# Optimization experiments

Hardware: AMD Instinct MI355X
Metric: run time of the kernel (lower is better)

## Reference

```python
import jax, jax.numpy as jnp
import numpy as np
from jax import lax

T, B, D_IN, H, D_OUT = 512, 64, 256, 512, 256


def _lstm_scan(xs, h0, c0, Wih, Whh, b):
    """Standard LSTM over time. xs: [T,B,Din]; returns (hs [T,B,H], hT, cT).
    Gate order i,f,g,o (PyTorch convention)."""
    def step(carry, x_t):
        h, c = carry
        gates = x_t @ Wih.T + h @ Whh.T + b            # [B, 4H]
        i, f, g, o = jnp.split(gates, 4, axis=-1)
        i = jax.nn.sigmoid(i)
        f = jax.nn.sigmoid(f)
        g = jnp.tanh(g)
        o = jax.nn.sigmoid(o)
        c = f * c + i * g
        h = o * jnp.tanh(c)
        return (h, c), h
    (hT, cT), hs = lax.scan(step, (h0, c0), xs)
    return hs, hT, cT


def setup_inputs() -> dict:
    key = jax.random.key(0)
    ks = jax.random.split(key, 10)
    s = 0.05
    return {
        "x": jax.random.normal(ks[0], (T, B, D_IN), jnp.float32),
        "target": jax.random.uniform(ks[1], (T, B, D_OUT), jnp.float32),
        "hidden_state": jnp.zeros((1, B, H), jnp.float32),
        "cell_state": jnp.zeros((1, B, H), jnp.float32),
        "enc_Wih": jax.random.normal(ks[2], (4 * H, D_IN), jnp.float32) * s,
        "enc_Whh": jax.random.normal(ks[3], (4 * H, H), jnp.float32) * s,
        "enc_b": jax.random.normal(ks[4], (4 * H,), jnp.float32) * s,
        "dec_Wih": jax.random.normal(ks[5], (4 * H, D_OUT), jnp.float32) * s,
        "dec_Whh": jax.random.normal(ks[6], (4 * H, H), jnp.float32) * s,
        "dec_b": jax.random.normal(ks[7], (4 * H,), jnp.float32) * s,
        "fc_W": jax.random.normal(ks[8], (D_OUT, H), jnp.float32) * s,
        "fc_b": jax.random.normal(ks[9], (D_OUT,), jnp.float32) * s,
    }


def reference(x, target, hidden_state, cell_state,
              enc_Wih, enc_Whh, enc_b, dec_Wih, dec_Whh, dec_b, fc_W, fc_b):
    # Encoder: consume x, keep final (h, c).
    _, h, c = _lstm_scan(x, hidden_state[0], cell_state[0], enc_Wih, enc_Whh, enc_b)
    # Decoder with teacher_forcing = 1.0: input at step t is target[t-1],
    # step 0 input is zeros (matches torch code's initial x = zeros).
    dec_in = jnp.concatenate([jnp.zeros((1,) + target.shape[1:], target.dtype),
                              target[:-1]], axis=0)          # [T, B, D_OUT]
    hs, _, _ = _lstm_scan(dec_in, h, c, dec_Wih, dec_Whh, dec_b)  # [T, B, H]
    logits = hs @ fc_W.T + fc_b                                   # [T, B, D_OUT]
    return jax.nn.softmax(logits, axis=-1)
```

## Files before the change

### kernel.cpp

```cpp
#include <hip/hip_runtime.h>
#include <math.h>

#define TT 512
#define BB 64
#define DIN 256
#define HH 512
#define DOUT 256

#define RSU 388
#define RSH 776
#define PST 68

#define A_HI_OFF 0
#define A_LO_OFF 6208
#define P_OFF    12416
#define B_OFF    14592
#define C_OFF    14656
#define HST_HI   14912
#define HST_LO   15040
#define SMEM_U32 15168
#define SMEM_BYTES (SMEM_U32*4)

#define FCS 516

typedef _Float16 f16x8 __attribute__((ext_vector_type(8)));
typedef float    f32x4 __attribute__((ext_vector_type(4)));
typedef unsigned u32x4 __attribute__((ext_vector_type(4)));

union H16 { _Float16 f; unsigned short u; };
__device__ __forceinline__ unsigned short f16bits(_Float16 h) { H16 t; t.f = h; return t.u; }

__device__ __forceinline__ void pack2(float x, float y, unsigned& hi, unsigned& lo) {
    _Float16 hx = (_Float16)x, hy = (_Float16)y;
    _Float16 lx = (_Float16)((x - (float)hx) * 2048.0f);
    _Float16 ly = (_Float16)((y - (float)hy) * 2048.0f);
    hi = (unsigned)f16bits(hx) | ((unsigned)f16bits(hy) << 16);
    lo = (unsigned)f16bits(lx) | ((unsigned)f16bits(ly) << 16);
}

__device__ __forceinline__ u32x4 ld16_cohere(const void* p) {
    u32x4 v;
    asm volatile("global_load_dwordx4 %0, %1, off sc0 sc1"
                 : "=&v"(v) : "v"(p) : "memory");
    return v;
}
__device__ __forceinline__ void st16_cohere(void* p, u32x4 v) {
    asm volatile("global_store_dwordx4 %0, %1, off sc0 sc1"
                 :: "v"(p), "v"(v) : "memory");
}

__device__ __forceinline__ bool tag_ok(u32x4 v, unsigned par) {
    unsigned a = v[0] & v[1] & v[2] & v[3];
    unsigned o = v[0] | v[1] | v[2] | v[3];
    unsigned x = par ? ~a : o;
    return (x & 0x00010001u) == 0u;
}

__device__ __forceinline__ void load_w_regs(const float* __restrict__ Whh,
                                            const float* __restrict__ Wih,
                                            int u0, int ct, int kh, int m, int q,
                                            f16x8 (&whi)[12], f16x8 (&wlo)[12]) {
    const int C = ct*HH + u0 + m;
    const float* rowH = Whh + (size_t)C*HH;
    const float* rowI = Wih + (size_t)C*DIN;
    #pragma unroll
    for (int j = 0; j < 12; ++j) {
        const int ks = kh*12 + j;
        const float* src = (ks < 16) ? (rowH + ks*32 + q*8)
                                     : (rowI + (ks - 16)*32 + q*8);
        float4 a = ((const float4*)src)[0];
        float4 b = ((const float4*)src)[1];
        f16x8 h8, l8; _Float16 t16;
        t16=(_Float16)a.x; h8[0]=t16; l8[0]=(_Float16)((a.x-(float)t16)*2048.0f);
        t16=(_Float16)a.y; h8[1]=t16; l8[1]=(_Float16)((a.y-(float)t16)*2048.0f);
        t16=(_Float16)a.z; h8[2]=t16; l8[2]=(_Float16)((a.z-(float)t16)*2048.0f);
        t16=(_Float16)a.w; h8[3]=t16; l8[3]=(_Float16)((a.w-(float)t16)*2048.0f);
        t16=(_Float16)b.x; h8[4]=t16; l8[4]=(_Float16)((b.x-(float)t16)*2048.0f);
        t16=(_Float16)b.y; h8[5]=t16; l8[5]=(_Float16)((b.y-(float)t16)*2048.0f);
        t16=(_Float16)b.z; h8[6]=t16; l8[6]=(_Float16)((b.z-(float)t16)*2048.0f);
        t16=(_Float16)b.w; h8[7]=t16; l8[7]=(_Float16)((b.w-(float)t16)*2048.0f);
        whi[j] = h8; wlo[j] = l8;
    }
}

__device__ __forceinline__ void stage_x_f16(unsigned* __restrict__ sm32,
                                            const float* __restrict__ src, int tid) {
    for (int r = 0; r < 2; ++r) {
        int idx4 = tid + 512*r;
        int b = idx4 >> 6, j4 = idx4 & 63;
        float4 v = ((const float4*)(src + (size_t)b*DIN))[j4];
        unsigned h0, l0, h1, l1;
        pack2(v.x, v.y, h0, l0);
        pack2(v.z, v.w, h1, l1);
        int o = b*RSU + 256 + 2*j4;
        sm32[A_HI_OFF + o]     = h0;
        sm32[A_HI_OFF + o + 1] = h1;
        sm32[A_LO_OFF + o]     = l0;
        sm32[A_LO_OFF + o + 1] = l1;
    }
}

__device__ __forceinline__ void stage_x_zero_f16(unsigned* __restrict__ sm32, int tid) {
    for (int r = 0; r < 2; ++r) {
        int idx = tid + 512*r;
        int row = idx >> 6, j = idx & 63;
        int o = row*RSU + 256 + 2*j;
        sm32[A_HI_OFF + o]     = 0u;
        sm32[A_HI_OFF + o + 1] = 0u;
        sm32[A_LO_OFF + o]     = 0u;
        sm32[A_LO_OFF + o + 1] = 0u;
    }
}

__global__ __launch_bounds__(512, 1)
void lstm_persist(const float* __restrict__ x, const float* __restrict__ target,
                  const float* __restrict__ h0, const float* __restrict__ c0,
                  const float* __restrict__ eWih, const float* __restrict__ eWhh,
                  const float* __restrict__ eb,
                  const float* __restrict__ dWih, const float* __restrict__ dWhh,
                  const float* __restrict__ db,
                  float* __restrict__ hs,
                  unsigned short* __restrict__ hbh,
                  unsigned short* __restrict__ hbl)
{
    extern __shared__ unsigned sm32[];
    float* p_l = (float*)(sm32 + P_OFF);
    float* b_l = (float*)(sm32 + B_OFF);
    float* c_l = (float*)(sm32 + C_OFF);
    unsigned* hst_hi = sm32 + HST_HI;
    unsigned* hst_lo = sm32 + HST_LO;

    const int tid = (int)threadIdx.x;
    const int g   = (int)(blockIdx.x & 3);
    const int ij  = (int)(blockIdx.x >> 2);
    const int b0  = g * 16;
    const int u0  = ij * 16;

    if (tid < 256) {
        int b = tid >> 4, u = tid & 15;
        c_l[tid] = c0[(size_t)(b0 + b)*HH + u0 + u];
    }
    if (tid < 64) b_l[tid] = eb[(tid >> 4)*HH + u0 + (tid & 15)];
    stage_x_f16(sm32, x + (size_t)b0*DIN, tid);
    for (int r = 0; r < 4; ++r) {
        int idx4 = tid + 512*r;
        int b = idx4 >> 7, j4 = idx4 & 127;
        float4 v = ((const float4*)(h0 + (size_t)(b0 + b)*HH))[j4];
        unsigned h0p, l0p, h1p, l1p;
        pack2(v.x, v.y, h0p, l0p);
        pack2(v.z, v.w, h1p, l1p);
        int o = b*RSU + 2*j4;
        sm32[A_HI_OFF + o]     = h0p;
        sm32[A_HI_OFF + o + 1] = h1p;
        sm32[A_LO_OFF + o]     = l0p;
        sm32[A_LO_OFF + o + 1] = l1p;
    }
    __syncthreads();

    const int lane = tid & 63;
    const int wid  = tid >> 6;
    const int m    = lane & 15;
    const int q    = lane >> 4;
    const int ct   = wid & 3;
    const int kh   = wid >> 2;

    const _Float16* aH = (const _Float16*)(sm32 + A_HI_OFF);
    const _Float16* aL = (const _Float16*)(sm32 + A_LO_OFF);
    const int abase = m*RSH + q*8 + (kh*12)*32;

    f16x8 whi[12], wlo[12];
    load_w_regs(eWhh, eWih, u0, ct, kh, m, q, whi, wlo);

    for (int s = 0; s < 1024; ++s) {
        f32x4 hh = {0.f,0.f,0.f,0.f}, hl = {0.f,0.f,0.f,0.f}, lh = {0.f,0.f,0.f,0.f};
        #pragma unroll
        for (int j = 0; j < 12; ++j) {
            f16x8 ah = *(const f16x8*)(aH + abase + j*32);
            f16x8 al = *(const f16x8*)(aL + abase + j*32);
            hh = __builtin_amdgcn_mfma_f32_16x16x32_f16(ah, whi[j], hh, 0, 0, 0);
            hl = __builtin_amdgcn_mfma_f32_16x16x32_f16(ah, wlo[j], hl, 0, 0, 0);
            lh = __builtin_amdgcn_mfma_f32_16x16x32_f16(al, whi[j], lh, 0, 0, 0);
        }
        {
            const float sc = 1.0f/2048.0f;
            float* pb = p_l + (kh*16 + q*4)*PST + ct*16 + m;
            #pragma unroll
            for (int i = 0; i < 4; ++i)
                pb[i*PST] = hh[i] + (hl[i] + lh[i])*sc;
        }
        __syncthreads();

        const unsigned par = (unsigned)(((s + 1) >> 1) & 1);

        float hval = 0.f;
        if (tid < 256) {
            const int b = tid >> 4, u = tid & 15;
            const float* p0 = p_l + (size_t)b*PST;
            const float* p1 = p_l + (size_t)(16 + b)*PST;
            float gi = b_l[u]      + p0[u]      + p1[u];
            float gf = b_l[16 + u] + p0[16 + u] + p1[16 + u];
            float gg = b_l[32 + u] + p0[32 + u] + p1[32 + u];
            float go = b_l[48 + u] + p0[48 + u] + p1[48 + u];
            float ii = 1.f/(1.f + expf(-gi));
            float ff = 1.f/(1.f + expf(-gf));
            float g2 = tanhf(gg);
            float oo = 1.f/(1.f + expf(-go));
            float c  = ff*c_l[tid] + ii*g2;
            c_l[tid] = c;
            hval = oo*tanhf(c);
            _Float16 hh16 = (_Float16)hval;
            unsigned uh = ((unsigned)f16bits(hh16) & 0xFFFEu) | par;
            H16 t16; t16.u = (unsigned short)uh;
            _Float16 hl16 = (_Float16)((hval - (float)t16.f) * 2048.0f);
            unsigned ul = ((unsigned)f16bits(hl16) & 0xFFFEu) | par;
            ((unsigned short*)hst_hi)[tid] = (unsigned short)uh;
            ((unsigned short*)hst_lo)[tid] = (unsigned short)ul;
        }
        __syncthreads();

        if (tid < 64) {
            asm volatile("s_waitcnt vmcnt(0)" ::: "memory");
            const int b = tid >> 2, part = tid & 3;
            const int isLo = part >> 1, h16 = part & 1;
            u32x4 v = *(const u32x4*)((isLo ? hst_lo : hst_hi) + b*8 + h16*4);
            unsigned short* base = (isLo ? hbl : hbh)
                + ((size_t)((s & 1) ^ 1)*BB + b0 + b)*HH + u0 + h16*8;
            st16_cohere(base, v);
        }

        if (s >= 512 && tid < 256) {
            int b = tid >> 4, u = tid & 15;
            hs[((size_t)(s - 512)*BB + (b0 + b))*HH + (u0 + u)] = hval;
        }
        if (s == 511) {
            load_w_regs(dWhh, dWih, u0, ct, kh, m, q, whi, wlo);
            if (tid < 64) b_l[tid] = db[(tid >> 4)*HH + u0 + (tid & 15)];
        }
        {
            int ns = s + 1;
            if (ns < 1024) {
                if (ns == 512)       stage_x_zero_f16(sm32, tid);
                else if (ns < 512)   stage_x_f16(sm32, x + ((size_t)ns*BB + b0)*DIN, tid);
                else                 stage_x_f16(sm32, target + ((size_t)(ns - 513)*BB + b0)*DOUT, tid);
            }
        }

        if (s < 1023) {
            const int slot = (s + 1) & 1;
            const u32x4* SH = (const u32x4*)(hbh + (size_t)slot*BB*HH + (size_t)b0*HH);
            const u32x4* SL = (const u32x4*)(hbl + (size_t)slot*BB*HH + (size_t)b0*HH);
            u32x4 v0 = {0,0,0,0}, v1 = {0,0,0,0}, v2 = {0,0,0,0}, v3 = {0,0,0,0};
            unsigned pend = 0xFu;
            do {
                if (pend & 1u) v0 = ld16_cohere(SH + tid);
                if (pend & 2u) v1 = ld16_cohere(SH + tid + 512);
                if (pend & 4u) v2 = ld16_cohere(SL + tid);
                if (pend & 8u) v3 = ld16_cohere(SL + tid + 512);
                asm volatile("s_waitcnt vmcnt(0)"
                             : "+v"(v0), "+v"(v1), "+v"(v2), "+v"(v3) :: "memory");
                if (tag_ok(v0, par)) pend &= ~1u;
                if (tag_ok(v1, par)) pend &= ~2u;
                if (tag_ok(v2, par)) pend &= ~4u;
                if (tag_ok(v3, par)) pend &= ~8u;
            } while (pend);
            const int j = tid & 63, r0 = tid >> 6;
            *(u32x4*)(sm32 + A_HI_OFF + (r0    )*RSU + j*4) = v0;
            *(u32x4*)(sm32 + A_HI_OFF + (r0 + 8)*RSU + j*4) = v1;
            *(u32x4*)(sm32 + A_LO_OFF + (r0    )*RSU + j*4) = v2;
            *(u32x4*)(sm32 + A_LO_OFF + (r0 + 8)*RSU + j*4) = v3;
        }
        __syncthreads();
    }
}

__global__ __launch_bounds__(256, 1)
void fc_kernel(const float* __restrict__ hs, const float* __restrict__ W,
               const float* __restrict__ bias, float* __restrict__ out)
{
    extern __shared__ float sm[];
    float* hs_l = sm;
    float* w_l  = sm + 16*FCS;

    const int tid = (int)threadIdx.x;
    const int rb = (int)(blockIdx.x >> 3);
    const int cb = (int)(blockIdx.x & 7);

    for (int r = 0; r < 8; ++r) {
        int id = tid + 256*r;
        int b = id >> 7, j = id & 127;
        float4 v = ((const float4*)(hs + (size_t)(rb*16 + b)*HH))[j];
        *(float4*)(hs_l + b*FCS + 4*j) = v;
    }
    for (int r = 0; r < 16; ++r) {
        int id = tid + 256*r;
        int c = id >> 7, j = id & 127;
        float4 v = ((const float4*)(W + (size_t)(cb*32 + c)*HH))[j];
        *(float4*)(w_l + c*FCS + 4*j) = v;
    }
    __syncthreads();

    const int kc = tid & 7, bt = (tid >> 3) & 3, ct = tid >> 5;
    float acc[4][4] = {};
    const float* ap = hs_l + (bt*4)*FCS + 4*kc;
    const float* wp = w_l  + (ct*4)*FCS + 4*kc;
    #pragma unroll 4
    for (int i = 0; i < 16; ++i) {
        float4 av[4], wv[4];
        #pragma unroll
        for (int q = 0; q < 4; ++q) av[q] = *(const float4*)(ap + q*FCS + 32*i);
        #pragma unroll
        for (int q = 0; q < 4; ++q) wv[q] = *(const float4*)(wp + q*FCS + 32*i);
        #pragma unroll
        for (int b2 = 0; b2 < 4; ++b2)
            #pragma unroll
            for (int c2 = 0; c2 < 4; ++c2)
                acc[b2][c2] += av[b2].x*wv[c2].x + av[b2].y*wv[c2].y
                             + av[b2].z*wv[c2].z + av[b2].w*wv[c2].w;
    }
    #pragma unroll
    for (int b2 = 0; b2 < 4; ++b2)
        #pragma unroll
        for (int c2 = 0; c2 < 4; ++c2) {
            float v = acc[b2][c2];
            v += __shfl_xor(v, 1, 64);
            v += __shfl_xor(v, 2, 64);
            v += __shfl_xor(v, 4, 64);
            acc[b2][c2] = v;
        }
    if (kc == 0) {
        #pragma unroll
        for (int b2 = 0; b2 < 4; ++b2)
            #pragma unroll
            for (int c2 = 0; c2 < 4; ++c2) {
                int row = rb*16 + bt*4 + b2;
                int col = cb*32 + ct*4 + c2;
                out[(size_t)row*DOUT + col] = acc[b2][c2] + bias[col];
            }
    }
}

__global__ __launch_bounds__(256, 1)
void softmax_kernel(float* __restrict__ out)
{
    int row  = (int)blockIdx.x * 4 + ((int)threadIdx.x >> 6);
    int lane = (int)threadIdx.x & 63;
    float4 v = ((const float4*)(out + (size_t)row*DOUT))[lane];
    float m = fmaxf(fmaxf(v.x, v.y), fmaxf(v.z, v.w));
    #pragma unroll
    for (int d = 1; d < 64; d <<= 1) m = fmaxf(m, __shfl_xor(m, d, 64));
    float ex = expf(v.x - m), ey = expf(v.y - m), ez = expf(v.z - m), ew = expf(v.w - m);
    float ssum = ex + ey + ez + ew;
    #pragma unroll
    for (int d = 1; d < 64; d <<= 1) ssum += __shfl_xor(ssum, d, 64);
    float inv = 1.f / ssum;
    float4 o = make_float4(ex*inv, ey*inv, ez*inv, ew*inv);
    ((float4*)(out + (size_t)row*DOUT))[lane] = o;
}

__global__ void init_kernel(unsigned* __restrict__ hbh32, unsigned* __restrict__ hbl32)
{
    int i = (int)blockIdx.x * 256 + (int)threadIdx.x;
    unsigned* base = (i < 8192) ? hbh32 : hbl32;
    int j = (i & 8191) * 4;
    unsigned val = (j < 16384) ? 0u : 0x00010001u;
    u32x4 v = {val, val, val, val};
    st16_cohere(base + j, v);
}

extern "C" void kernel_launch(void* const* d_in, const int* in_sizes, int n_in,
                              void* d_out, int out_size, void* d_ws, size_t ws_size,
                              hipStream_t stream) {
    (void)in_sizes; (void)n_in; (void)out_size; (void)ws_size;
    const float* x      = (const float*)d_in[0];
    const float* target = (const float*)d_in[1];
    const float* h0     = (const float*)d_in[2];
    const float* c0     = (const float*)d_in[3];
    const float* eWih   = (const float*)d_in[4];
    const float* eWhh   = (const float*)d_in[5];
    const float* eb     = (const float*)d_in[6];
    const float* dWih   = (const float*)d_in[7];
    const float* dWhh   = (const float*)d_in[8];
    const float* db     = (const float*)d_in[9];
    const float* fcW    = (const float*)d_in[10];
    const float* fcb    = (const float*)d_in[11];
    float* out = (float*)d_out;

    float* hs = (float*)d_ws + 1024;
    unsigned short* hbh = (unsigned short*)(hs + (size_t)TT*BB*HH);
    unsigned short* hbl = hbh + (size_t)2*BB*HH;

    init_kernel<<<dim3(64), dim3(256), 0, stream>>>((unsigned*)hbh, (unsigned*)hbl);

    lstm_persist<<<dim3(128), dim3(512), SMEM_BYTES, stream>>>(
        x, target, h0, c0, eWih, eWhh, eb, dWih, dWhh, db, hs, hbh, hbl);

    size_t lds_fc = (size_t)(48*FCS) * sizeof(float);
    fc_kernel<<<dim3(16384), dim3(256), lds_fc, stream>>>(hs, fcW, fcb, out);

    softmax_kernel<<<dim3(8192), dim3(256), 0, stream>>>(out);
}
```

Baseline: 4.013 ms.

## Overlap input-projection MFMAs with cross-block hidden-state wait; shuffle-based h publish

Reorders the per-step K split so each wave first runs the MFMAs for the x-input columns, which do not depend on the previous hidden state. Only then does it spin on the cross-block hidden-state exchange and run the recurrent columns. This hides part of the inter-block synchronisation latency behind independent tensor work. The hidden-state publish now packs values with wave shuffles and stores straight from registers, removing an LDS staging buffer and one __syncthreads per step. The restructured barrier placement and the parity handling must stay correct across blocks.

Measured after the change: 4.173 ms. +4.0%, slower.

```diff
diff --git a/kernel.cpp b/kernel.cpp
--- a/kernel.cpp
+++ b/kernel.cpp
@@ -16,9 +16,7 @@
 #define P_OFF    12416
 #define B_OFF    14592
 #define C_OFF    14656
-#define HST_HI   14912
-#define HST_LO   15040
-#define SMEM_U32 15168
+#define SMEM_U32 14912
 #define SMEM_BYTES (SMEM_U32*4)
 
 #define FCS 516
@@ -64,8 +62,8 @@
     const float* rowH = Whh + (size_t)C*HH;
     const float* rowI = Wih + (size_t)C*DIN;
     #pragma unroll
-    for (int j = 0; j < 12; ++j) {
-        const int ks = kh*12 + j;
+    for (int jj = 0; jj < 12; ++jj) {
+        const int ks = (jj < 8) ? (kh*8 + jj) : (16 + kh*4 + (jj - 8));
         const float* src = (ks < 16) ? (rowH + ks*32 + q*8)
                                      : (rowI + (ks - 16)*32 + q*8);
         float4 a = ((const float4*)src)[0];
@@ -79,7 +77,7 @@
         t16=(_Float16)b.y; h8[5]=t16; l8[5]=(_Float16)((b.y-(float)t16)*2048.0f);
         t16=(_Float16)b.z; h8[6]=t16; l8[6]=(_Float16)((b.z-(float)t16)*2048.0f);
         t16=(_Float16)b.w; h8[7]=t16; l8[7]=(_Float16)((b.w-(float)t16)*2048.0f);
-        whi[j] = h8; wlo[j] = l8;
+        whi[jj] = h8; wlo[jj] = l8;
     }
 }
 
@@ -127,8 +125,6 @@
     float* p_l = (float*)(sm32 + P_OFF);
     float* b_l = (float*)(sm32 + B_OFF);
     float* c_l = (float*)(sm32 + C_OFF);
-    unsigned* hst_hi = sm32 + HST_HI;
-    unsigned* hst_lo = sm32 + HST_LO;
 
     const int tid = (int)threadIdx.x;
     const int g   = (int)(blockIdx.x & 3);
@@ -166,7 +162,7 @@
 
     const _Float16* aH = (const _Float16*)(sm32 + A_HI_OFF);
     const _Float16* aL = (const _Float16*)(sm32 + A_LO_OFF);
-    const int abase = m*RSH + q*8 + (kh*12)*32;
+    const int abase = m*RSH + q*8;
 
     f16x8 whi[12], wlo[12];
     load_w_regs(eWhh, eWih, u0, ct, kh, m, q, whi, wlo);
@@ -174,12 +170,50 @@
     for (int s = 0; s < 1024; ++s) {
         f32x4 hh = {0.f,0.f,0.f,0.f}, hl = {0.f,0.f,0.f,0.f}, lh = {0.f,0.f,0.f,0.f};
         #pragma unroll
-        for (int j = 0; j < 12; ++j) {
-            f16x8 ah = *(const f16x8*)(aH + abase + j*32);
-            f16x8 al = *(const f16x8*)(aL + abase + j*32);
-            hh = __builtin_amdgcn_mfma_f32_16x16x32_f16(ah, whi[j], hh, 0, 0, 0);
-            hl = __builtin_amdgcn_mfma_f32_16x16x32_f16(ah, wlo[j], hl, 0, 0, 0);
-            lh = __builtin_amdgcn_mfma_f32_16x16x32_f16(al, whi[j], lh, 0, 0, 0);
+        for (int jj = 8; jj < 12; ++jj) {
+            const int ks = 16 + kh*4 + (jj - 8);
+            f16x8 ah = *(const f16x8*)(aH + abase + ks*32);
+            f16x8 al = *(const f16x8*)(aL + abase + ks*32);
+            hh = __builtin_amdgcn_mfma_f32_16x16x32_f16(ah, whi[jj], hh, 0, 0, 0);
+            hl = __builtin_amdgcn_mfma_f32_16x16x32_f16(ah, wlo[jj], hl, 0, 0, 0);
+            lh = __builtin_amdgcn_mfma_f32_16x16x32_f16(al, whi[jj], lh, 0, 0, 0);
+        }
+
+        if (s > 0) {
+            const int slot = s & 1;
+            const unsigned par2 = (unsigned)((s >> 1) & 1);
+            const u32x4* SH = (const u32x4*)(hbh + (size_t)slot*BB*HH + (size_t)b0*HH);
+            const u32x4* SL = (const u32x4*)(hbl + (size_t)slot*BB*HH + (size_t)b0*HH);
+            u32x4 v0 = {0,0,0,0}, v1 = {0,0,0,0}, v2 = {0,0,0,0}, v3 = {0,0,0,0};
+            unsigned pend = 0xFu;
+            do {
+                if (pend & 1u) v0 = ld16_cohere(SH + tid);
+                if (pend & 2u) v1 = ld16_cohere(SH + tid + 512);
+                if (pend & 4u) v2 = ld16_cohere(SL + tid);
+                if (pend & 8u) v3 = ld16_cohere(SL + tid + 512);
+                asm volatile("s_waitcnt vmcnt(0)"
+                             : "+v"(v0), "+v"(v1), "+v"(v2), "+v"(v3) :: "memory");
+                if (tag_ok(v0, par2)) pend &= ~1u;
+                if (tag_ok(v1, par2)) pend &= ~2u;
+                if (tag_ok(v2, par2)) pend &= ~4u;
+                if (tag_ok(v3, par2)) pend &= ~8u;
+            } while (pend);
+            const int j = tid & 63, r0 = tid >> 6;
+            *(u32x4*)(sm32 + A_HI_OFF + (r0    )*RSU + j*4) = v0;
+            *(u32x4*)(sm32 + A_HI_OFF + (r0 + 8)*RSU + j*4) = v1;
+            *(u32x4*)(sm32 + A_LO_OFF + (r0    )*RSU + j*4) = v2;
+            *(u32x4*)(sm32 + A_LO_OFF + (r0 + 8)*RSU + j*4) = v3;
+            __syncthreads();
+        }
+
+        #pragma unroll
+        for (int jj = 0; jj < 8; ++jj) {
+            const int ks = kh*8 + jj;
+            f16x8 ah = *(const f16x8*)(aH + abase + ks*32);
+            f16x8 al = *(const f16x8*)(aL + abase + ks*32);
+            hh = __builtin_amdgcn_mfma_f32_16x16x32_f16(ah, whi[jj], hh, 0, 0, 0);
+            hl = __builtin_amdgcn_mfma_f32_16x16x32_f16(ah, wlo[jj], hl, 0, 0, 0);
+            lh = __builtin_amdgcn_mfma_f32_16x16x32_f16(al, whi[jj], lh, 0, 0, 0);
         }
         {
             const float sc = 1.0f/2048.0f;
@@ -213,19 +247,22 @@
             H16 t16; t16.u = (unsigned short)uh;
             _Float16 hl16 = (_Float16)((hval - (float)t16.f) * 2048.0f);
             unsigned ul = ((unsigned)f16bits(hl16) & 0xFFFEu) | par;
-            ((unsigned short*)hst_hi)[tid] = (unsigned short)uh;
-            ((unsigned short*)hst_lo)[tid] = (unsigned short)ul;
-        }
-        __syncthreads();
-
-        if (tid < 64) {
+
             asm volatile("s_waitcnt vmcnt(0)" ::: "memory");
-            const int b = tid >> 2, part = tid & 3;
-            const int isLo = part >> 1, h16 = part & 1;
-            u32x4 v = *(const u32x4*)((isLo ? hst_lo : hst_hi) + b*8 + h16*4);
-            unsigned short* base = (isLo ? hbl : hbh)
-                + ((size_t)((s & 1) ^ 1)*BB + b0 + b)*HH + u0 + h16*8;
-            st16_cohere(base, v);
+            unsigned r0h = uh | (__shfl_xor(uh, 1, 64) << 16);
+            unsigned r0l = ul | (__shfl_xor(ul, 1, 64) << 16);
+            u32x4 vh, vl;
+            vh[0] = r0h; vh[1] = __shfl_xor(r0h, 2, 64);
+            vh[2] = __shfl_xor(r0h, 4, 64); vh[3] = __shfl_xor(r0h, 6, 64);
+            vl[0] = r0l; vl[1] = __shfl_xor(r0l, 2, 64);
+            vl[2] = __shfl_xor(r0l, 4, 64); vl[3] = __shfl_xor(r0l, 6, 64);
+            if ((u & 7) == 0) {
+                const int h16 = u >> 3;
+                size_t off = (size_t)((s & 1) ^ 1)*BB*HH
+                           + (size_t)(b0 + b)*HH + u0 + h16*8;
+                st16_cohere(hbh + off, vh);
+                st16_cohere(hbl + off, vl);
+            }
         }
 
         if (s >= 512 && tid < 256) {
@@ -243,31 +280,6 @@
                 else if (ns < 512)   stage_x_f16(sm32, x + ((size_t)ns*BB + b0)*DIN, tid);
                 else                 stage_x_f16(sm32, target + ((size_t)(ns - 513)*BB + b0)*DOUT, tid);
             }
-        }
-
-        if (s < 1023) {
-            const int slot = (s + 1) & 1;
-            const u32x4* SH = (const u32x4*)(hbh + (size_t)slot*BB*HH + (size_t)b0*HH);
-            const u32x4* SL = (const u32x4*)(hbl + (size_t)slot*BB*HH + (size_t)b0*HH);
-            u32x4 v0 = {0,0,0,0}, v1 = {0,0,0,0}, v2 = {0,0,0,0}, v3 = {0,0,0,0};
-            unsigned pend = 0xFu;
-            do {
-                if (pend & 1u) v0 = ld16_cohere(SH + tid);
-                if (pend & 2u) v1 = ld16_cohere(SH + tid + 512);
-                if (pend & 4u) v2 = ld16_cohere(SL + tid);
-                if (pend & 8u) v3 = ld16_cohere(SL + tid + 512);
-                asm volatile("s_waitcnt vmcnt(0)"
-                             : "+v"(v0), "+v"(v1), "+v"(v2), "+v"(v3) :: "memory");
-                if (tag_ok(v0, par)) pend &= ~1u;
-                if (tag_ok(v1, par)) pend &= ~2u;
-                if (tag_ok(v2, par)) pend &= ~4u;
-                if (tag_ok(v3, par)) pend &= ~8u;
-            } while (pend);
-            const int j = tid & 63, r0 = tid >> 6;
-            *(u32x4*)(sm32 + A_HI_OFF + (r0    )*RSU + j*4) = v0;
-            *(u32x4*)(sm32 + A_HI_OFF + (r0 + 8)*RSU + j*4) = v1;
-            *(u32x4*)(sm32 + A_LO_OFF + (r0    )*RSU + j*4) = v2;
-            *(u32x4*)(sm32 + A_LO_OFF + (r0 + 8)*RSU + j*4) = v3;
         }
         __syncthreads();
     }
```

## Load recurrent h directly into MFMA operands from global, overlapping x-projection with wait

Applied to the files above, without the earlier changes.

Each wave is repartitioned to cover all four gates over a slice of the K dimension. The wave now polls the tagged h exchange buffer from global memory straight into MFMA operand registers and consumes each half as soon as it is ready, instead of having the whole block wait, copy into LDS and sync. The x-input projection is issued before the poll so it overlaps the cross-block wait. The hi*lo MFMA products are folded into one accumulator, h0 initialisation moves into the init kernel, and the gate reduction now sums eight partials instead of two. The risk is extra wave-level spinning and global-load latency sitting on the critical path of every step.

Measured after the change: 4.358 ms. +8.6%, slower.

```diff
diff --git a/kernel.cpp b/kernel.cpp
--- a/kernel.cpp
+++ b/kernel.cpp
@@ -7,18 +7,18 @@
 #define HH 512
 #define DOUT 256
 
-#define RSU 388
-#define RSH 776
-#define PST 68
-
-#define A_HI_OFF 0
-#define A_LO_OFF 6208
-#define P_OFF    12416
-#define B_OFF    14592
-#define C_OFF    14656
-#define HST_HI   14912
-#define HST_LO   15040
-#define SMEM_U32 15168
+#define RSXU 132
+#define RSXH 264
+#define PST  68
+
+#define AXH_OFF 0
+#define AXL_OFF 2112
+#define P_OFF   4224
+#define B_OFF   12928
+#define C_OFF   12992
+#define HST_HI  13248
+#define HST_LO  13376
+#define SMEM_U32 13504
 #define SMEM_BYTES (SMEM_U32*4)
 
 #define FCS 516
@@ -27,7 +27,8 @@
 typedef float    f32x4 __attribute__((ext_vector_type(4)));
 typedef unsigned u32x4 __attribute__((ext_vector_type(4)));
 
-union H16 { _Float16 f; unsigned short u; };
+union H16  { _Float16 f; unsigned short u; };
+union V16  { u32x4 u; f16x8 f; };
 __device__ __forceinline__ unsigned short f16bits(_Float16 h) { H16 t; t.f = h; return t.u; }
 
 __device__ __forceinline__ void pack2(float x, float y, unsigned& hi, unsigned& lo) {
@@ -48,6 +49,10 @@
     asm volatile("global_store_dwordx4 %0, %1, off sc0 sc1"
                  :: "v"(p), "v"(v) : "memory");
 }
+__device__ __forceinline__ void st32_cohere(unsigned* p, unsigned v) {
+    asm volatile("global_store_dword %0, %1, off sc0 sc1"
+                 :: "v"(p), "v"(v) : "memory");
+}
 
 __device__ __forceinline__ bool tag_ok(u32x4 v, unsigned par) {
     unsigned a = v[0] & v[1] & v[2] & v[3];
@@ -58,28 +63,30 @@
 
 __device__ __forceinline__ void load_w_regs(const float* __restrict__ Whh,
                                             const float* __restrict__ Wih,
-                                            int u0, int ct, int kh, int m, int q,
-                                            f16x8 (&whi)[12], f16x8 (&wlo)[12]) {
-    const int C = ct*HH + u0 + m;
-    const float* rowH = Whh + (size_t)C*HH;
-    const float* rowI = Wih + (size_t)C*DIN;
+                                            int u0, int w, int m, int q,
+                                            f16x8 (&whi)[4][3], f16x8 (&wlo)[4][3]) {
     #pragma unroll
-    for (int j = 0; j < 12; ++j) {
-        const int ks = kh*12 + j;
-        const float* src = (ks < 16) ? (rowH + ks*32 + q*8)
-                                     : (rowI + (ks - 16)*32 + q*8);
-        float4 a = ((const float4*)src)[0];
-        float4 b = ((const float4*)src)[1];
-        f16x8 h8, l8; _Float16 t16;
-        t16=(_Float16)a.x; h8[0]=t16; l8[0]=(_Float16)((a.x-(float)t16)*2048.0f);
-        t16=(_Float16)a.y; h8[1]=t16; l8[1]=(_Float16)((a.y-(float)t16)*2048.0f);
-        t16=(_Float16)a.z; h8[2]=t16; l8[2]=(_Float16)((a.z-(float)t16)*2048.0f);
-        t16=(_Float16)a.w; h8[3]=t16; l8[3]=(_Float16)((a.w-(float)t16)*2048.0f);
-        t16=(_Float16)b.x; h8[4]=t16; l8[4]=(_Float16)((b.x-(float)t16)*2048.0f);
-        t16=(_Float16)b.y; h8[5]=t16; l8[5]=(_Float16)((b.y-(float)t16)*2048.0f);
-        t16=(_Float16)b.z; h8[6]=t16; l8[6]=(_Float16)((b.z-(float)t16)*2048.0f);
-        t16=(_Float16)b.w; h8[7]=t16; l8[7]=(_Float16)((b.w-(float)t16)*2048.0f);
-        whi[j] = h8; wlo[j] = l8;
+    for (int g = 0; g < 4; ++g) {
+        const int C = g*HH + u0 + m;
+        const float* rowH = Whh + (size_t)C*HH;
+        const float* rowI = Wih + (size_t)C*DIN;
+        #pragma unroll
+        for (int sl = 0; sl < 3; ++sl) {
+            const float* src = (sl < 2) ? (rowH + (2*w + sl)*32 + q*8)
+                                        : (rowI + w*32 + q*8);
+            float4 a = ((const float4*)src)[0];
+            float4 b = ((const float4*)src)[1];
+            f16x8 h8, l8; _Float16 t16;
+            t16=(_Float16)a.x; h8[0]=t16; l8[0]=(_Float16)((a.x-(float)t16)*2048.0f);
+            t16=(_Float16)a.y; h8[1]=t16; l8[1]=(_Float16)((a.y-(float)t16)*2048.0f);
+            t16=(_Float16)a.z; h8[2]=t16; l8[2]=(_Float16)((a.z-(float)t16)*2048.0f);
+            t16=(_Float16)a.w; h8[3]=t16; l8[3]=(_Float16)((a.w-(float)t16)*2048.0f);
+            t16=(_Float16)b.x; h8[4]=t16; l8[4]=(_Float16)((b.x-(float)t16)*2048.0f);
+            t16=(_Float16)b.y; h8[5]=t16; l8[5]=(_Float16)((b.y-(float)t16)*2048.0f);
+            t16=(_Float16)b.z; h8[6]=t16; l8[6]=(_Float16)((b.z-(float)t16)*2048.0f);
+            t16=(_Float16)b.w; h8[7]=t16; l8[7]=(_Float16)((b.w-(float)t16)*2048.0f);
+            whi[g][sl] = h8; wlo[g][sl] = l8;
+        }
     }
 }
 
@@ -92,11 +99,11 @@
         unsigned h0, l0, h1, l1;
         pack2(v.x, v.y, h0, l0);
         pack2(v.z, v.w, h1, l1);
-        int o = b*RSU + 256 + 2*j4;
-        sm32[A_HI_OFF + o]     = h0;
-        sm32[A_HI_OFF + o + 1] = h1;
-        sm32[A_LO_OFF + o]     = l0;
-        sm32[A_LO_OFF + o + 1] = l1;
+        int o = b*RSXU + 2*j4;
+        sm32[AXH_OFF + o]     = h0;
+        sm32[AXH_OFF + o + 1] = h1;
+        sm32[AXL_OFF + o]     = l0;
+        sm32[AXL_OFF + o + 1] = l1;
     }
 }
 
@@ -104,17 +111,17 @@
     for (int r = 0; r < 2; ++r) {
         int idx = tid + 512*r;
         int row = idx >> 6, j = idx & 63;
-        int o = row*RSU + 256 + 2*j;
-        sm32[A_HI_OFF + o]     = 0u;
-        sm32[A_HI_OFF + o + 1] = 0u;
-        sm32[A_LO_OFF + o]     = 0u;
-        sm32[A_LO_OFF + o + 1] = 0u;
+        int o = row*RSXU + 2*j;
+        sm32[AXH_OFF + o]     = 0u;
+        sm32[AXH_OFF + o + 1] = 0u;
+        sm32[AXL_OFF + o]     = 0u;
+        sm32[AXL_OFF + o + 1] = 0u;
     }
 }
 
 __global__ __launch_bounds__(512, 1)
 void lstm_persist(const float* __restrict__ x, const float* __restrict__ target,
-                  const float* __restrict__ h0, const float* __restrict__ c0,
+                  const float* __restrict__ c0,
                   const float* __restrict__ eWih, const float* __restrict__ eWhh,
                   const float* __restrict__ eb,
                   const float* __restrict__ dWih, const float* __restrict__ dWhh,
@@ -142,77 +149,117 @@
     }
     if (tid < 64) b_l[tid] = eb[(tid >> 4)*HH + u0 + (tid & 15)];
     stage_x_f16(sm32, x + (size_t)b0*DIN, tid);
-    for (int r = 0; r < 4; ++r) {
-        int idx4 = tid + 512*r;
-        int b = idx4 >> 7, j4 = idx4 & 127;
-        float4 v = ((const float4*)(h0 + (size_t)(b0 + b)*HH))[j4];
-        unsigned h0p, l0p, h1p, l1p;
-        pack2(v.x, v.y, h0p, l0p);
-        pack2(v.z, v.w, h1p, l1p);
-        int o = b*RSU + 2*j4;
-        sm32[A_HI_OFF + o]     = h0p;
-        sm32[A_HI_OFF + o + 1] = h1p;
-        sm32[A_LO_OFF + o]     = l0p;
-        sm32[A_LO_OFF + o + 1] = l1p;
-    }
     __syncthreads();
 
     const int lane = tid & 63;
     const int wid  = tid >> 6;
     const int m    = lane & 15;
     const int q    = lane >> 4;
-    const int ct   = wid & 3;
-    const int kh   = wid >> 2;
-
-    const _Float16* aH = (const _Float16*)(sm32 + A_HI_OFF);
-    const _Float16* aL = (const _Float16*)(sm32 + A_LO_OFF);
-    const int abase = m*RSH + q*8 + (kh*12)*32;
-
-    f16x8 whi[12], wlo[12];
-    load_w_regs(eWhh, eWih, u0, ct, kh, m, q, whi, wlo);
+
+    f16x8 whi[4][3], wlo[4][3];
+    load_w_regs(eWhh, eWih, u0, wid, m, q, whi, wlo);
+
+    const _Float16* aXH = (const _Float16*)(sm32 + AXH_OFF);
+    const _Float16* aXL = (const _Float16*)(sm32 + AXL_OFF);
+    const int xoff = m*RSXH + wid*32 + q*8;
+    const int o0 = wid*64 + q*8;
+    const int o1 = o0 + 32;
 
     for (int s = 0; s < 1024; ++s) {
-        f32x4 hh = {0.f,0.f,0.f,0.f}, hl = {0.f,0.f,0.f,0.f}, lh = {0.f,0.f,0.f,0.f};
-        #pragma unroll
-        for (int j = 0; j < 12; ++j) {
-            f16x8 ah = *(const f16x8*)(aH + abase + j*32);
-            f16x8 al = *(const f16x8*)(aL + abase + j*32);
-            hh = __builtin_amdgcn_mfma_f32_16x16x32_f16(ah, whi[j], hh, 0, 0, 0);
-            hl = __builtin_amdgcn_mfma_f32_16x16x32_f16(ah, wlo[j], hl, 0, 0, 0);
-            lh = __builtin_amdgcn_mfma_f32_16x16x32_f16(al, whi[j], lh, 0, 0, 0);
-        }
+        const int gslot = s & 1;
+        const unsigned gpar = (unsigned)((s >> 1) & 1);
+
+        f32x4 ahh[4], alo[4];
+        #pragma unroll
+        for (int gg = 0; gg < 4; ++gg) {
+            ahh[gg] = (f32x4){0.f,0.f,0.f,0.f};
+            alo[gg] = (f32x4){0.f,0.f,0.f,0.f};
+        }
+
+        {
+            f16x8 xh = *(const f16x8*)(aXH + xoff);
+            f16x8 xl = *(const f16x8*)(aXL + xoff);
+            #pragma unroll
+            for (int gg = 0; gg < 4; ++gg) {
+                ahh[gg] = __builtin_amdgcn_mfma_f32_16x16x32_f16(xh, whi[gg][2], ahh[gg], 0, 0, 0);
+                alo[gg] = __builtin_amdgcn_mfma_f32_16x16x32_f16(xl, whi[gg][2],
+                          __builtin_amdgcn_mfma_f32_16x16x32_f16(xh, wlo[gg][2], alo[gg], 0, 0, 0), 0, 0, 0);
+            }
+        }
+
+        {
+            const unsigned short* SH = hbh + (size_t)gslot*BB*HH + (size_t)(b0 + m)*HH;
+            const unsigned short* SL = hbl + (size_t)gslot*BB*HH + (size_t)(b0 + m)*HH;
+            u32x4 a0h = {0,0,0,0}, a0l = {0,0,0,0}, a1h = {0,0,0,0}, a1l = {0,0,0,0};
+            unsigned lp = 3u;
+            unsigned wp = 3u;
+            do {
+                if (lp & 1u) { a0h = ld16_cohere(SH + o0); a0l = ld16_cohere(SL + o0); }
+                if (lp & 2u) { a1h = ld16_cohere(SH + o1); a1l = ld16_cohere(SL + o1); }
+                asm volatile("s_waitcnt vmcnt(0)"
+                             : "+v"(a0h), "+v"(a0l), "+v"(a1h), "+v"(a1l) :: "memory");
+                if ((lp & 1u) && tag_ok(a0h, gpar) && tag_ok(a0l, gpar)) lp &= ~1u;
+                if ((lp & 2u) && tag_ok(a1h, gpar) && tag_ok(a1l, gpar)) lp &= ~2u;
+                if ((wp & 1u) && __all((lp & 1u) == 0u)) {
+                    V16 vh, vl; vh.u = a0h; vl.u = a0l;
+                    #pragma unroll
+                    for (int gg = 0; gg < 4; ++gg) {
+                        ahh[gg] = __builtin_amdgcn_mfma_f32_16x16x32_f16(vh.f, whi[gg][0], ahh[gg], 0, 0, 0);
+                        alo[gg] = __builtin_amdgcn_mfma_f32_16x16x32_f16(vl.f, whi[gg][0],
+                                  __builtin_amdgcn_mfma_f32_16x16x32_f16(vh.f, wlo[gg][0], alo[gg], 0, 0, 0), 0, 0, 0);
+                    }
+                    wp &= ~1u;
+                }
+                if ((wp & 2u) && __all((lp & 2u) == 0u)) {
+                    V16 vh, vl; vh.u = a1h; vl.u = a1l;
+                    #pragma unroll
+                    for (int gg = 0; gg < 4; ++gg) {
+                        ahh[gg] = __builtin_amdgcn_mfma_f32_16x16x32_f16(vh.f, whi[gg][1], ahh[gg], 0, 0, 0);
+                        alo[gg] = __builtin_amdgcn_mfma_f32_16x16x32_f16(vl.f, whi[gg][1],
+                                  __builtin_amdgcn_mfma_f32_16x16x32_f16(vh.f, wlo[gg][1], alo[gg], 0, 0, 0), 0, 0, 0);
+                    }
+                    wp &= ~2u;
+                }
+            } while (wp);
+        }
+
         {
             const float sc = 1.0f/2048.0f;
-            float* pb = p_l + (kh*16 + q*4)*PST + ct*16 + m;
+            float* pb = p_l + (wid*16 + q*4)*PST + m;
             #pragma unroll
-            for (int i = 0; i < 4; ++i)
-                pb[i*PST] = hh[i] + (hl[i] + lh[i])*sc;
+            for (int gg = 0; gg < 4; ++gg)
+                #pragma unroll
+                for (int i = 0; i < 4; ++i)
+                    pb[i*PST + gg*16] = ahh[gg][i] + alo[gg][i]*sc;
         }
         __syncthreads();
 
-        const unsigned par = (unsigned)(((s + 1) >> 1) & 1);
+        const unsigned ppar = (unsigned)(((s + 1) >> 1) & 1);
 
         float hval = 0.f;
         if (tid < 256) {
             const int b = tid >> 4, u = tid & 15;
-            const float* p0 = p_l + (size_t)b*PST;
-            const float* p1 = p_l + (size_t)(16 + b)*PST;
-            float gi = b_l[u]      + p0[u]      + p1[u];
-            float gf = b_l[16 + u] + p0[16 + u] + p1[16 + u];
-            float gg = b_l[32 + u] + p0[32 + u] + p1[32 + u];
-            float go = b_l[48 + u] + p0[48 + u] + p1[48 + u];
+            float gi = b_l[u], gf = b_l[16 + u], gg2 = b_l[32 + u], go = b_l[48 + u];
+            #pragma unroll
+            for (int w = 0; w < 8; ++w) {
+                const float* pp = p_l + (size_t)(w*16 + b)*PST;
+                gi  += pp[u];
+                gf  += pp[16 + u];
+                gg2 += pp[32 + u];
+                go  += pp[48 + u];
+            }
             float ii = 1.f/(1.f + expf(-gi));
             float ff = 1.f/(1.f + expf(-gf));
-            float g2 = tanhf(gg);
+            float g2 = tanhf(gg2);
             float oo = 1.f/(1.f + expf(-go));
             float c  = ff*c_l[tid] + ii*g2;
             c_l[tid] = c;
             hval = oo*tanhf(c);
             _Float16 hh16 = (_Float16)hval;
-            unsigned uh = ((unsigned)f16bits(hh16) & 0xFFFEu) | par;
+            unsigned uh = ((unsigned)f16bits(hh16) & 0xFFFEu) | ppar;
             H16 t16; t16.u = (unsigned short)uh;
             _Float16 hl16 = (_Float16)((hval - (float)t16.f) * 2048.0f);
-            unsigned ul = ((unsigned)f16bits(hl16) & 0xFFFEu) | par;
+            unsigned ul = ((unsigned)f16bits(hl16) & 0xFFFEu) | ppar;
             ((unsigned short*)hst_hi)[tid] = (unsigned short)uh;
             ((unsigned short*)hst_lo)[tid] = (unsigned short)ul;
         }
@@ -233,7 +280,7 @@
             hs[((size_t)(s - 512)*BB + (b0 + b))*HH + (u0 + u)] = hval;
         }
         if (s == 511) {
-            load_w_regs(dWhh, dWih, u0, ct, kh, m, q, whi, wlo);
+            load_w_regs(dWhh, dWih, u0, wid, m, q, whi, wlo);
             if (tid < 64) b_l[tid] = db[(tid >> 4)*HH + u0 + (tid & 15)];
         }
         {
@@ -243,31 +290,6 @@
                 else if (ns < 512)   stage_x_f16(sm32, x + ((size_t)ns*BB + b0)*DIN, tid);
                 else                 stage_x_f16(sm32, target + ((size_t)(ns - 513)*BB + b0)*DOUT, tid);
             }
-        }
-
-        if (s < 1023) {
-            const int slot = (s + 1) & 1;
-            const u32x4* SH = (const u32x4*)(hbh + (size_t)slot*BB*HH + (size_t)b0*HH);
-            const u32x4* SL = (const u32x4*)(hbl + (size_t)slot*BB*HH + (size_t)b0*HH);
-            u32x4 v0 = {0,0,0,0}, v1 = {0,0,0,0}, v2 = {0,0,0,0}, v3 = {0,0,0,0};
-            unsigned pend = 0xFu;
-            do {
-                if (pend & 1u) v0 = ld16_cohere(SH + tid);
-                if (pend & 2u) v1 = ld16_cohere(SH + tid + 512);
-                if (pend & 4u) v2 = ld16_cohere(SL + tid);
-                if (pend & 8u) v3 = ld16_cohere(SL + tid + 512);
-                asm volatile("s_waitcnt vmcnt(0)"
-                             : "+v"(v0), "+v"(v1), "+v"(v2), "+v"(v3) :: "memory");
-                if (tag_ok(v0, par)) pend &= ~1u;
-                if (tag_ok(v1, par)) pend &= ~2u;
-                if (tag_ok(v2, par)) pend &= ~4u;
-                if (tag_ok(v3, par)) pend &= ~8u;
-            } while (pend);
-            const int j = tid & 63, r0 = tid >> 6;
-            *(u32x4*)(sm32 + A_HI_OFF + (r0    )*RSU + j*4) = v0;
-            *(u32x4*)(sm32 + A_HI_OFF + (r0 + 8)*RSU + j*4) = v1;
-            *(u32x4*)(sm32 + A_LO_OFF + (r0    )*RSU + j*4) = v2;
-            *(u32x4*)(sm32 + A_LO_OFF + (r0 + 8)*RSU + j*4) = v3;
         }
         __syncthreads();
     }
@@ -357,14 +379,23 @@
     ((float4*)(out + (size_t)row*DOUT))[lane] = o;
 }
 
-__global__ void init_kernel(unsigned* __restrict__ hbh32, unsigned* __restrict__ hbl32)
+__global__ void init_kernel(const float* __restrict__ h0,
+                            unsigned* __restrict__ hbh32, unsigned* __restrict__ hbl32)
 {
     int i = (int)blockIdx.x * 256 + (int)threadIdx.x;
-    unsigned* base = (i < 8192) ? hbh32 : hbl32;
-    int j = (i & 8191) * 4;
-    unsigned val = (j < 16384) ? 0u : 0x00010001u;
-    u32x4 v = {val, val, val, val};
-    st16_cohere(base + j, v);
+    float x0 = h0[2*i], x1 = h0[2*i + 1];
+    _Float16 ha = (_Float16)x0;
+    unsigned ua = (unsigned)f16bits(ha) & 0xFFFEu;
+    H16 ta; ta.u = (unsigned short)ua;
+    unsigned la = (unsigned)f16bits((_Float16)((x0 - (float)ta.f)*2048.0f)) & 0xFFFEu;
+    _Float16 hb = (_Float16)x1;
+    unsigned ub = (unsigned)f16bits(hb) & 0xFFFEu;
+    H16 tb; tb.u = (unsigned short)ub;
+    unsigned lb = (unsigned)f16bits((_Float16)((x1 - (float)tb.f)*2048.0f)) & 0xFFFEu;
+    st32_cohere(hbh32 + i, ua | (ub << 16));
+    st32_cohere(hbl32 + i, la | (lb << 16));
+    st32_cohere(hbh32 + 16384 + i, 0x00010001u);
+    st32_cohere(hbl32 + 16384 + i, 0x00010001u);
 }
 
 extern "C" void kernel_launch(void* const* d_in, const int* in_sizes, int n_in,
@@ -389,10 +420,10 @@
     unsigned short* hbh = (unsigned short*)(hs + (size_t)TT*BB*HH);
     unsigned short* hbl = hbh + (size_t)2*BB*HH;
 
-    init_kernel<<<dim3(64), dim3(256), 0, stream>>>((unsigned*)hbh, (unsigned*)hbl);
+    init_kernel<<<dim3(64), dim3(256), 0, stream>>>(h0, (unsigned*)hbh, (unsigned*)hbl);
 
     lstm_persist<<<dim3(128), dim3(512), SMEM_BYTES, stream>>>(
-        x, target, h0, c0, eWih, eWhh, eb, dWih, dWhh, db, hs, hbh, hbl);
+        x, target, c0, eWih, eWhh, eb, dWih, dWhh, db, hs, hbh, hbl);
 
     size_t lds_fc = (size_t)(48*FCS) * sizeof(float);
     fc_kernel<<<dim3(16384), dim3(256), lds_fc, stream>>>(hs, fcW, fcb, out);
```
